# Kernel tuning notes

Measured on AMD Instinct MI355X. Metric: run time of the kernel, lower is better.

The kernel has to match this reference:

```python
import jax, jax.numpy as jnp
import numpy as np

N, E = 100000, 3200000
EMB, HID, OUT = 128, 16, 32
NEG = 0.2  # GATv2 default negative_slope


def _w(key, shape, fan_in):
    return (jax.random.normal(key, shape, jnp.float32) / np.sqrt(fan_in)).astype(jnp.float32)


def setup_inputs() -> dict:
    key = jax.random.key(0)
    ks = jax.random.split(key, 16)
    x = jax.random.normal(ks[0], (N, EMB), jnp.float32)
    edge_index = jax.random.randint(ks[1], (2, E), 0, N, dtype=jnp.int64)
    edge_attr = jax.random.normal(ks[2], (E, 1), jnp.float32)
    return {
        "x": x, "edge_index": edge_index, "edge_attr": edge_attr,
        # layer1: GATv2Conv(EMB -> HID, heads=1, edge_dim=1)
        "W1l": _w(ks[3], (EMB, HID), EMB), "W1r": _w(ks[4], (EMB, HID), EMB),
        "W1e": _w(ks[5], (1, HID), 1), "att1": _w(ks[6], (HID,), HID),
        "b1": jnp.zeros((HID,), jnp.float32),
        # layer2: GATv2Conv(HID -> OUT, heads=1, edge_dim=1)
        "W2l": _w(ks[7], (HID, OUT), HID), "W2r": _w(ks[8], (HID, OUT), HID),
        "W2e": _w(ks[9], (1, OUT), 1), "att2": _w(ks[10], (OUT,), OUT),
        "b2": jnp.zeros((OUT,), jnp.float32),
    }


def gatv2_layer(x, ei, ea, Wl, Wr, We, att, b):
    """PyG GATv2Conv, heads=1, add_self_loops=True (edge fill_value='mean')."""
    n = x.shape[0]
    loop = jnp.arange(n, dtype=ei.dtype)
    ei = jnp.concatenate([ei, jnp.stack([loop, loop])], axis=1)          # [2, E+n]
    ea = jnp.concatenate(
        [ea, jnp.broadcast_to(ea.mean(0, keepdims=True), (n, ea.shape[1]))], axis=0)
    src, dst = ei[0], ei[1]
    xl = x @ Wl                                                          # source proj
    xr = x @ Wr                                                          # target proj
    h = jax.nn.leaky_relu(xl[src] + xr[dst] + ea @ We, NEG)              # [E', C]
    logits = h @ att                                                     # [E']
    m = jax.ops.segment_max(logits, dst, num_segments=n)                 # per-dst softmax
    ex = jnp.exp(logits - m[dst])
    denom = jax.ops.segment_sum(ex, dst, num_segments=n)
    alpha = ex / denom[dst]                                              # [E']
    out = jax.ops.segment_sum(alpha[:, None] * xl[src], dst, num_segments=n) + b
    return out, ei, alpha[:, None]


def reference(x, edge_index, edge_attr, W1l, W1r, W1e, att1, b1, W2l, W2r, W2e, att2, b2):
    h, ei1, a1 = gatv2_layer(x, edge_index, edge_attr, W1l, W1r, W1e, att1, b1)
    h = jax.nn.relu(h)  # F.dropout with training=False is identity (eval mode)
    out, ei2, a2 = gatv2_layer(h, ei1, a1, W2l, W2r, W2e, att2, b2)
    return out, ei2, a2
```

## Files before the change

kernel.cpp:

```cpp
#include <hip/hip_runtime.h>

#define DEVFN __device__ __forceinline__

constexpr int GN = 100000, GE = 3200000;
constexpr int GE1 = GE + GN;
constexpr int GE2 = GE1 + GN;
constexpr int GEMB = 128, GHID = 16, GOUT = 32;
constexpr float GNEG = 0.2f;
constexpr float GEA2 = 100000.f / 3300000.f;

constexpr long long G0 = (long long)GN * GOUT;
constexpr long long G1 = G0 + 2LL * GE2;

constexpr unsigned CHUNK = 400000;

constexpr size_t W_ESC  = 0;
constexpr size_t W_XL1H = 3400000;
constexpr size_t W_XR1  = 4200000;
constexpr size_t W_XL2H = 5800000;
constexpr size_t W_XR2  = 7400000;
constexpr size_t W_RP   = 10600000;
constexpr size_t W_CNT  = 10700004;
constexpr size_t W_BS   = 10800004;
constexpr size_t W_SEA  = 10800260;
constexpr size_t W_WPI  = 10800261;
constexpr size_t W_END  = 10800264;

DEVFN int gidx(const int* __restrict__ ei, long long i, int wpi) {
    return ei[(size_t)i * (size_t)wpi];
}
DEVFN unsigned short f2b(float f) {
    unsigned u = __float_as_uint(f);
    unsigned r = ((u >> 16) & 1u) + 0x7fffu;
    return (unsigned short)((u + r) >> 16);
}
DEVFN float b2fl(unsigned u) { return __uint_as_float(u << 16); }
DEVFN float b2fh(unsigned u) { return __uint_as_float(u & 0xffff0000u); }

__global__ void gl_sentinel(float* outb) {
    if (threadIdx.x == 0 && blockIdx.x == 0) outb[G1] = 3840.0f;
}

__global__ void gl_detect(const int* __restrict__ ei, int* flag) {
    int t = threadIdx.x;
    int v = ei[2 * t + 1];
    unsigned long long nz = __ballot(v != 0);
    if (t == 0) *flag = (nz == 0ull) ? 2 : 1;
}

__global__ void gl_sum(const float* __restrict__ p, int n, float* __restrict__ out) {
    float s = 0.f;
    for (int i = blockIdx.x * blockDim.x + threadIdx.x; i < n; i += gridDim.x * blockDim.x)
        s += p[i];
    #pragma unroll
    for (int o = 32; o > 0; o >>= 1) s += __shfl_down(s, o);
    __shared__ float ls[4];
    if ((threadIdx.x & 63) == 0) ls[threadIdx.x >> 6] = s;
    __syncthreads();
    if (threadIdx.x == 0) atomicAdd(out, ls[0] + ls[1] + ls[2] + ls[3]);
}

__global__ __launch_bounds__(256) void gl_projA(const float* __restrict__ x,
        const float* __restrict__ Wl, const float* __restrict__ Wr,
        unsigned short* __restrict__ xlh, float* __restrict__ xr) {
    __shared__ float sWl[GEMB * GHID], sWr[GEMB * GHID], sx[16 * GEMB];
    for (int i = threadIdx.x; i < GEMB * GHID; i += 256) { sWl[i] = Wl[i]; sWr[i] = Wr[i]; }
    int base = blockIdx.x * 16;
    for (int i = threadIdx.x; i < 16 * GEMB; i += 256) sx[i] = x[(size_t)base * GEMB + i];
    __syncthreads();
    int ln = threadIdx.x >> 4, ch = threadIdx.x & 15;
    float al = 0.f, ar = 0.f;
    #pragma unroll 8
    for (int k = 0; k < GEMB; ++k) {
        float xv = sx[ln * GEMB + k];
        al = fmaf(xv, sWl[k * GHID + ch], al);
        ar = fmaf(xv, sWr[k * GHID + ch], ar);
    }
    xlh[(size_t)(base + ln) * GHID + ch] = f2b(al);
    xr[(size_t)(base + ln) * GHID + ch] = ar;
}

__global__ __launch_bounds__(256) void gl_projB(const float* __restrict__ h,
        const float* __restrict__ Wl, const float* __restrict__ Wr,
        unsigned short* __restrict__ xlh, float* __restrict__ xr) {
    __shared__ float sWl[GHID * GOUT], sWr[GHID * GOUT], sx[8 * GHID];
    for (int i = threadIdx.x; i < GHID * GOUT; i += 256) { sWl[i] = Wl[i]; sWr[i] = Wr[i]; }
    int base = blockIdx.x * 8;
    for (int i = threadIdx.x; i < 8 * GHID; i += 256) sx[i] = h[(size_t)base * GHID + i];
    __syncthreads();
    int ln = threadIdx.x >> 5, ch = threadIdx.x & 31;
    float al = 0.f, ar = 0.f;
    #pragma unroll
    for (int k = 0; k < GHID; ++k) {
        float xv = sx[ln * GHID + k];
        al = fmaf(xv, sWl[k * GOUT + ch], al);
        ar = fmaf(xv, sWr[k * GOUT + ch], ar);
    }
    xlh[(size_t)(base + ln) * GOUT + ch] = f2b(al);
    xr[(size_t)(base + ln) * GOUT + ch] = ar;
}

__global__ void gl_hist(const int* __restrict__ ei, const int* __restrict__ wpip,
                        int* __restrict__ cnt, int2* __restrict__ dl) {
    int e = blockIdx.x * blockDim.x + threadIdx.x;
    if (e >= GE) return;
    int wpi = *wpip;
    int dst = gidx(ei, (long long)GE + e, wpi);
    int lc = atomicAdd(&cnt[dst], 1);
    dl[e] = make_int2(dst, lc);
}

__global__ __launch_bounds__(1024) void gl_scan1(const int* __restrict__ cnt,
                                                 int* __restrict__ rp, int* __restrict__ bs) {
    __shared__ int s[1024];
    int t = threadIdx.x, u = blockIdx.x * 1024 + t;
    s[t] = (u < GN) ? cnt[u] : 0;
    __syncthreads();
    for (int off = 1; off < 1024; off <<= 1) {
        int a = (t >= off) ? s[t - off] : 0;
        __syncthreads();
        s[t] += a;
        __syncthreads();
    }
    if (u < GN) rp[u + 1] = s[t];
    if (t == 1023) bs[blockIdx.x] = s[1023];
}
__global__ void gl_scan2(int* __restrict__ bs, int nb) {
    __shared__ int s[128];
    int t = threadIdx.x;
    s[t] = (t < nb) ? bs[t] : 0;
    __syncthreads();
    for (int off = 1; off < 128; off <<= 1) {
        int a = (t >= off) ? s[t - off] : 0;
        __syncthreads();
        s[t] += a;
        __syncthreads();
    }
    if (t < nb) bs[t] = (t == 0) ? 0 : s[t - 1];
}
__global__ void gl_scan3(int* __restrict__ rp, const int* __restrict__ bs) {
    int u = blockIdx.x * blockDim.x + threadIdx.x;
    if (u < GN) rp[u + 1] += bs[u >> 10];
    if (u == 0) rp[0] = 0;
}

__global__ void gl_slots(const int2* __restrict__ dl, const int* __restrict__ rp,
                         int* __restrict__ inv) {
    int e = blockIdx.x * blockDim.x + threadIdx.x;
    if (e >= GE) return;
    int2 d = dl[e];
    inv[e] = rp[d.x] + d.y;
}

__global__ __launch_bounds__(256) void gl_scatter(const int* __restrict__ ei,
        const int* __restrict__ wpip, const float* __restrict__ eattr,
        const int* __restrict__ inv, int2* __restrict__ pse) {
    int wpi = *wpip;
    unsigned ck = blockIdx.x & 7;
    int stride = (gridDim.x >> 3) * 256;
    for (int e = (blockIdx.x >> 3) * 256 + threadIdx.x; e < GE; e += stride) {
        int slot = inv[e];
        if ((unsigned)slot / CHUNK == ck) {
            int src = gidx(ei, e, wpi);
            pse[slot] = make_int2(src, __float_as_int(eattr[e]));
        }
    }
}

__global__ __launch_bounds__(256) void gl_L1(const int* __restrict__ rp,
        const int2* __restrict__ pse, const float* __restrict__ sea,
        const unsigned short* __restrict__ xlh, const float* __restrict__ xr,
        const float* __restrict__ We, const float* __restrict__ att,
        const float* __restrict__ b1, float* __restrict__ esc,
        float* __restrict__ h1) {
    int u = blockIdx.x * 4 + (threadIdx.x >> 6);
    int lane = threadIdx.x & 63, sg = lane >> 2, ln4 = lane & 3;
    int beg = rp[u], end = rp[u + 1];
    float4 we = *(const float4*)(We + ln4 * 4);
    float4 at = *(const float4*)(att + ln4 * 4);
    float4 xru = *(const float4*)(xr + (size_t)u * GHID + ln4 * 4);
    float mx = -3.0e38f, pd = 0.f;
    float4 acc = make_float4(0.f, 0.f, 0.f, 0.f);
    for (int i = beg + sg; i < end; i += 16) {
        int2 p = pse[i];
        uint2 h = *(const uint2*)(xlh + (size_t)p.x * GHID + ln4 * 4);
        float ea = __int_as_float(p.y);
        float x0 = b2fl(h.x), x1 = b2fh(h.x), x2 = b2fl(h.y), x3 = b2fh(h.y);
        float v, s = 0.f;
        v = x0 + xru.x + ea * we.x; v = v > 0.f ? v : GNEG * v; s = fmaf(v, at.x, s);
        v = x1 + xru.y + ea * we.y; v = v > 0.f ? v : GNEG * v; s = fmaf(v, at.y, s);
        v = x2 + xru.z + ea * we.z; v = v > 0.f ? v : GNEG * v; s = fmaf(v, at.z, s);
        v = x3 + xru.w + ea * we.w; v = v > 0.f ? v : GNEG * v; s = fmaf(v, at.w, s);
        s += __shfl_xor(s, 1); s += __shfl_xor(s, 2);
        if (ln4 == 0) esc[i] = s;
        float nm = fmaxf(mx, s);
        float sc = __expf(mx - nm), pp = __expf(s - nm);
        pd = pd * sc + pp;
        acc.x = acc.x * sc + pp * x0; acc.y = acc.y * sc + pp * x1;
        acc.z = acc.z * sc + pp * x2; acc.w = acc.w * sc + pp * x3;
        mx = nm;
    }
    float lgself = 0.f;
    if (sg == 0) {
        uint2 h = *(const uint2*)(xlh + (size_t)u * GHID + ln4 * 4);
        float ea = sea[0] * (1.f / (float)GE);
        float x0 = b2fl(h.x), x1 = b2fh(h.x), x2 = b2fl(h.y), x3 = b2fh(h.y);
        float v, s = 0.f;
        v = x0 + xru.x + ea * we.x; v = v > 0.f ? v : GNEG * v; s = fmaf(v, at.x, s);
        v = x1 + xru.y + ea * we.y; v = v > 0.f ? v : GNEG * v; s = fmaf(v, at.y, s);
        v = x2 + xru.z + ea * we.z; v = v > 0.f ? v : GNEG * v; s = fmaf(v, at.z, s);
        v = x3 + xru.w + ea * we.w; v = v > 0.f ? v : GNEG * v; s = fmaf(v, at.w, s);
        s += __shfl_xor(s, 1); s += __shfl_xor(s, 2);
        lgself = s;
        float nm = fmaxf(mx, s);
        float sc = __expf(mx - nm), pp = __expf(s - nm);
        pd = pd * sc + pp;
        acc.x = acc.x * sc + pp * x0; acc.y = acc.y * sc + pp * x1;
        acc.z = acc.z * sc + pp * x2; acc.w = acc.w * sc + pp * x3;
        mx = nm;
    }
    #pragma unroll
    for (int o = 4; o <= 32; o <<= 1) {
        float mo = __shfl_xor(mx, o), po = __shfl_xor(pd, o);
        float a0 = __shfl_xor(acc.x, o), a1 = __shfl_xor(acc.y, o);
        float a2 = __shfl_xor(acc.z, o), a3 = __shfl_xor(acc.w, o);
        float nm = fmaxf(mx, mo);
        float sa = __expf(mx - nm), sb = __expf(mo - nm);
        pd = pd * sa + po * sb;
        acc.x = acc.x * sa + a0 * sb; acc.y = acc.y * sa + a1 * sb;
        acc.z = acc.z * sa + a2 * sb; acc.w = acc.w * sa + a3 * sb;
        mx = nm;
    }
    float dinv = 1.f / pd;
    __threadfence_block();
    for (int i = beg + lane; i < end; i += 64)
        esc[i] = __expf(esc[i] - mx) * dinv;
    if (lane == 0) esc[GE + u] = __expf(lgself - mx) * dinv;
    if (lane < 4) {
        float4 b = *(const float4*)(b1 + lane * 4);
        float4 o;
        o.x = acc.x * dinv + b.x; o.y = acc.y * dinv + b.y;
        o.z = acc.z * dinv + b.z; o.w = acc.w * dinv + b.w;
        o.x = o.x > 0.f ? o.x : 0.f; o.y = o.y > 0.f ? o.y : 0.f;
        o.z = o.z > 0.f ? o.z : 0.f; o.w = o.w > 0.f ? o.w : 0.f;
        *(float4*)(h1 + (size_t)u * GHID + lane * 4) = o;
    }
}

__global__ __launch_bounds__(256) void gl_L2(const int* __restrict__ rp,
        const int2* __restrict__ pse,
        const unsigned short* __restrict__ xlh, const float* __restrict__ xr,
        const float* __restrict__ We, const float* __restrict__ att,
        const float* __restrict__ b2, float* __restrict__ esc,
        float* __restrict__ out0) {
    int u = blockIdx.x * 4 + (threadIdx.x >> 6);
    int lane = threadIdx.x & 63, sg = lane >> 3, ln8 = lane & 7;
    int beg = rp[u], end = rp[u + 1];
    float4 we = *(const float4*)(We + ln8 * 4);
    float4 at = *(const float4*)(att + ln8 * 4);
    float4 xru = *(const float4*)(xr + (size_t)u * GOUT + ln8 * 4);
    float mx = -3.0e38f, pd = 0.f;
    float4 acc = make_float4(0.f, 0.f, 0.f, 0.f);
    for (int i = beg + sg; i < end; i += 8) {
        int2 p = pse[i];
        float ea = esc[i];
        uint2 h = *(const uint2*)(xlh + (size_t)p.x * GOUT + ln8 * 4);
        float x0 = b2fl(h.x), x1 = b2fh(h.x), x2 = b2fl(h.y), x3 = b2fh(h.y);
        float v, s = 0.f;
        v = x0 + xru.x + ea * we.x; v = v > 0.f ? v : GNEG * v; s = fmaf(v, at.x, s);
        v = x1 + xru.y + ea * we.y; v = v > 0.f ? v : GNEG * v; s = fmaf(v, at.y, s);
        v = x2 + xru.z + ea * we.z; v = v > 0.f ? v : GNEG * v; s = fmaf(v, at.z, s);
        v = x3 + xru.w + ea * we.w; v = v > 0.f ? v : GNEG * v; s = fmaf(v, at.w, s);
        s += __shfl_xor(s, 1); s += __shfl_xor(s, 2); s += __shfl_xor(s, 4);
        if (ln8 == 0) esc[i] = s;
        float nm = fmaxf(mx, s);
        float sc = __expf(mx - nm), pp = __expf(s - nm);
        pd = pd * sc + pp;
        acc.x = acc.x * sc + pp * x0; acc.y = acc.y * sc + pp * x1;
        acc.z = acc.z * sc + pp * x2; acc.w = acc.w * sc + pp * x3;
        mx = nm;
    }
    float lgs = 0.f;
    if (sg < 2) {
        float ea = (sg == 0) ? esc[GE + u] : GEA2;
        uint2 h = *(const uint2*)(xlh + (size_t)u * GOUT + ln8 * 4);
        float x0 = b2fl(h.x), x1 = b2fh(h.x), x2 = b2fl(h.y), x3 = b2fh(h.y);
        float v, s = 0.f;
        v = x0 + xru.x + ea * we.x; v = v > 0.f ? v : GNEG * v; s = fmaf(v, at.x, s);
        v = x1 + xru.y + ea * we.y; v = v > 0.f ? v : GNEG * v; s = fmaf(v, at.y, s);
        v = x2 + xru.z + ea * we.z; v = v > 0.f ? v : GNEG * v; s = fmaf(v, at.z, s);
        v = x3 + xru.w + ea * we.w; v = v > 0.f ? v : GNEG * v; s = fmaf(v, at.w, s);
        s += __shfl_xor(s, 1); s += __shfl_xor(s, 2); s += __shfl_xor(s, 4);
        lgs = s;
        float nm = fmaxf(mx, s);
        float sc = __expf(mx - nm), pp = __expf(s - nm);
        pd = pd * sc + pp;
        acc.x = acc.x * sc + pp * x0; acc.y = acc.y * sc + pp * x1;
        acc.z = acc.z * sc + pp * x2; acc.w = acc.w * sc + pp * x3;
        mx = nm;
    }
    #pragma unroll
    for (int o = 8; o <= 32; o <<= 1) {
        float mo = __shfl_xor(mx, o), po = __shfl_xor(pd, o);
        float a0 = __shfl_xor(acc.x, o), a1 = __shfl_xor(acc.y, o);
        float a2 = __shfl_xor(acc.z, o), a3 = __shfl_xor(acc.w, o);
        float nm = fmaxf(mx, mo);
        float sa = __expf(mx - nm), sb = __expf(mo - nm);
        pd = pd * sa + po * sb;
        acc.x = acc.x * sa + a0 * sb; acc.y = acc.y * sa + a1 * sb;
        acc.z = acc.z * sa + a2 * sb; acc.w = acc.w * sa + a3 * sb;
        mx = nm;
    }
    float dinv = 1.f / pd;
    __threadfence_block();
    for (int i = beg + lane; i < end; i += 64)
        esc[i] = __expf(esc[i] - mx) * dinv;
    if (lane == 0) esc[GE + u]  = __expf(lgs - mx) * dinv;
    if (lane == 8) esc[GE1 + u] = __expf(lgs - mx) * dinv;
    if (lane < 8) {
        float4 b = *(const float4*)(b2 + lane * 4);
        float4 o;
        o.x = acc.x * dinv + b.x; o.y = acc.y * dinv + b.y;
        o.z = acc.z * dinv + b.z; o.w = acc.w * dinv + b.w;
        *(float4*)(out0 + (size_t)u * GOUT + lane * 4) = o;
    }
}

__global__ void gl_ep(const int* __restrict__ ei, const int* __restrict__ wpip,
                      const int* __restrict__ inv, const float* __restrict__ esc,
                      float* __restrict__ outb) {
    int c = blockIdx.x * blockDim.x + threadIdx.x;
    if (c >= GE2) return;
    int wpi = *wpip;
    int s, dd;
    float av;
    if (c < GE) {
        s = gidx(ei, c, wpi);
        dd = gidx(ei, (long long)GE + c, wpi);
        av = esc[inv[c]];
    } else if (c < GE1) {
        s = dd = c - GE;
        av = esc[c];
    } else {
        s = dd = c - GE1;
        av = esc[c];
    }
    outb[G0 + c]       = (float)s;
    outb[G0 + GE2 + c] = (float)dd;
    outb[G1 + c]       = av;
}

extern "C" void kernel_launch(void* const* d_in, const int* in_sizes, int n_in,
                              void* d_out, int out_size, void* d_ws, size_t ws_size,
                              hipStream_t stream) {
    const float* x     = (const float*)d_in[0];
    const int*   ei    = (const int*)d_in[1];
    const float* eattr = (const float*)d_in[2];
    const float* W1l   = (const float*)d_in[3];
    const float* W1r   = (const float*)d_in[4];
    const float* W1e   = (const float*)d_in[5];
    const float* att1  = (const float*)d_in[6];
    const float* b1    = (const float*)d_in[7];
    const float* W2l   = (const float*)d_in[8];
    const float* W2r   = (const float*)d_in[9];
    const float* W2e   = (const float*)d_in[10];
    const float* att2  = (const float*)d_in[11];
    const float* b2    = (const float*)d_in[12];
    float* outf = (float*)d_out;

    float* ws = (float*)d_ws;
    if (W_END * sizeof(float) > ws_size) {
        gl_sentinel<<<1, 64, 0, stream>>>(outf);
        return;
    }

    float*          esc  = ws + W_ESC;
    unsigned short* xl1h = (unsigned short*)(ws + W_XL1H);
    float*          xr1  = ws + W_XR1;
    unsigned short* xl2h = (unsigned short*)(ws + W_XL2H);
    float*          xr2  = ws + W_XR2;
    int*            rp   = (int*)(ws + W_RP);
    int*            cnt  = (int*)(ws + W_CNT);
    int*            bs   = (int*)(ws + W_BS);
    float*          sea  = ws + W_SEA;
    int*            wpi  = (int*)(ws + W_WPI);

    int2*  dl  = (int2*)(outf + G0);
    int2*  pse = (int2*)(outf + G0);
    int*   inv = (int*)(outf + G1);
    float* h1  = outf;

    hipMemsetAsync(cnt, 0, GN * sizeof(int), stream);
    hipMemsetAsync(sea, 0, 2 * sizeof(float), stream);

    gl_detect<<<1, 64, 0, stream>>>(ei, wpi);
    gl_sum<<<1024, 256, 0, stream>>>(eattr, GE, sea);
    gl_projA<<<GN / 16, 256, 0, stream>>>(x, W1l, W1r, xl1h, xr1);

    int nbe = (GE + 255) / 256;
    gl_hist<<<nbe, 256, 0, stream>>>(ei, wpi, cnt, dl);
    gl_scan1<<<(GN + 1023) / 1024, 1024, 0, stream>>>(cnt, rp, bs);
    gl_scan2<<<1, 128, 0, stream>>>(bs, (GN + 1023) / 1024);
    gl_scan3<<<(GN + 255) / 256, 256, 0, stream>>>(rp, bs);
    gl_slots<<<nbe, 256, 0, stream>>>(dl, rp, inv);
    gl_scatter<<<8192, 256, 0, stream>>>(ei, wpi, eattr, inv, pse);

    gl_L1<<<GN / 4, 256, 0, stream>>>(rp, pse, sea, xl1h, xr1, W1e, att1, b1, esc, h1);
    gl_projB<<<GN / 8, 256, 0, stream>>>(h1, W2l, W2r, xl2h, xr2);
    gl_L2<<<GN / 4, 256, 0, stream>>>(rp, pse, xl2h, xr2, W2e, att2, b2, esc, outf);
    gl_ep<<<(GE2 + 255) / 256, 256, 0, stream>>>(ei, wpi, inv, esc, outf);
}
```

Baseline: 524.2 us.

## Prefetch next edge records in aggregation loops and shrink histogram side buffer

The per-destination aggregation loops in both layers now load the next edge's (src, attr) pair, and in layer 2 the next edge attribute, one iteration ahead. This is meant to hide gather latency behind the current edge's compute. Raw logits now go to a separate workspace buffer instead of being written to and reread from esc in place, which the layer-2 prefetch of esc needs. The histogram pass stores only a rank per edge instead of a (dst, rank) pair, and the slot pass rereads dst from edge_index, trading a smaller write for an extra strided read.

Result: no change. 516.6 us (-1.4%).

```diff
diff --git a/kernel.cpp b/kernel.cpp
--- a/kernel.cpp
+++ b/kernel.cpp
@@ -15,16 +15,17 @@
 constexpr unsigned CHUNK = 400000;
 
 constexpr size_t W_ESC  = 0;
-constexpr size_t W_XL1H = 3400000;
-constexpr size_t W_XR1  = 4200000;
-constexpr size_t W_XL2H = 5800000;
-constexpr size_t W_XR2  = 7400000;
-constexpr size_t W_RP   = 10600000;
-constexpr size_t W_CNT  = 10700004;
-constexpr size_t W_BS   = 10800004;
-constexpr size_t W_SEA  = 10800260;
-constexpr size_t W_WPI  = 10800261;
-constexpr size_t W_END  = 10800264;
+constexpr size_t W_LG   = 3400000;
+constexpr size_t W_XL1H = 6800000;
+constexpr size_t W_XR1  = 7600000;
+constexpr size_t W_XL2H = 9200000;
+constexpr size_t W_XR2  = 10800000;
+constexpr size_t W_RP   = 14000000;
+constexpr size_t W_CNT  = 14100004;
+constexpr size_t W_BS   = 14200004;
+constexpr size_t W_SEA  = 14200260;
+constexpr size_t W_WPI  = 14200261;
+constexpr size_t W_END  = 14200264;
 
 DEVFN int gidx(const int* __restrict__ ei, long long i, int wpi) {
     return ei[(size_t)i * (size_t)wpi];
@@ -101,13 +102,12 @@
 }
 
 __global__ void gl_hist(const int* __restrict__ ei, const int* __restrict__ wpip,
-                        int* __restrict__ cnt, int2* __restrict__ dl) {
+                        int* __restrict__ cnt, int* __restrict__ rank) {
     int e = blockIdx.x * blockDim.x + threadIdx.x;
     if (e >= GE) return;
     int wpi = *wpip;
     int dst = gidx(ei, (long long)GE + e, wpi);
-    int lc = atomicAdd(&cnt[dst], 1);
-    dl[e] = make_int2(dst, lc);
+    rank[e] = atomicAdd(&cnt[dst], 1);
 }
 
 __global__ __launch_bounds__(1024) void gl_scan1(const int* __restrict__ cnt,
@@ -144,12 +144,14 @@
     if (u == 0) rp[0] = 0;
 }
 
-__global__ void gl_slots(const int2* __restrict__ dl, const int* __restrict__ rp,
+__global__ void gl_slots(const int* __restrict__ ei, const int* __restrict__ wpip,
+                         const int* __restrict__ rank, const int* __restrict__ rp,
                          int* __restrict__ inv) {
     int e = blockIdx.x * blockDim.x + threadIdx.x;
     if (e >= GE) return;
-    int2 d = dl[e];
-    inv[e] = rp[d.x] + d.y;
+    int wpi = *wpip;
+    int dst = gidx(ei, (long long)GE + e, wpi);
+    inv[e] = rp[dst] + rank[e];
 }
 
 __global__ __launch_bounds__(256) void gl_scatter(const int* __restrict__ ei,
@@ -172,7 +174,7 @@
         const unsigned short* __restrict__ xlh, const float* __restrict__ xr,
         const float* __restrict__ We, const float* __restrict__ att,
         const float* __restrict__ b1, float* __restrict__ esc,
-        float* __restrict__ h1) {
+        float* __restrict__ lg, float* __restrict__ h1) {
     int u = blockIdx.x * 4 + (threadIdx.x >> 6);
     int lane = threadIdx.x & 63, sg = lane >> 2, ln4 = lane & 3;
     int beg = rp[u], end = rp[u + 1];
@@ -181,8 +183,11 @@
     float4 xru = *(const float4*)(xr + (size_t)u * GHID + ln4 * 4);
     float mx = -3.0e38f, pd = 0.f;
     float4 acc = make_float4(0.f, 0.f, 0.f, 0.f);
-    for (int i = beg + sg; i < end; i += 16) {
-        int2 p = pse[i];
+    int i = beg + sg;
+    int2 p = (i < end) ? pse[i] : make_int2(0, 0);
+    for (; i < end; i += 16) {
+        int inx = i + 16;
+        int2 pn = (inx < end) ? pse[inx] : make_int2(0, 0);
         uint2 h = *(const uint2*)(xlh + (size_t)p.x * GHID + ln4 * 4);
         float ea = __int_as_float(p.y);
         float x0 = b2fl(h.x), x1 = b2fh(h.x), x2 = b2fl(h.y), x3 = b2fh(h.y);
@@ -192,13 +197,14 @@
         v = x2 + xru.z + ea * we.z; v = v > 0.f ? v : GNEG * v; s = fmaf(v, at.z, s);
         v = x3 + xru.w + ea * we.w; v = v > 0.f ? v : GNEG * v; s = fmaf(v, at.w, s);
         s += __shfl_xor(s, 1); s += __shfl_xor(s, 2);
-        if (ln4 == 0) esc[i] = s;
+        if (ln4 == 0) lg[i] = s;
         float nm = fmaxf(mx, s);
         float sc = __expf(mx - nm), pp = __expf(s - nm);
         pd = pd * sc + pp;
         acc.x = acc.x * sc + pp * x0; acc.y = acc.y * sc + pp * x1;
         acc.z = acc.z * sc + pp * x2; acc.w = acc.w * sc + pp * x3;
         mx = nm;
+        p = pn;
     }
     float lgself = 0.f;
     if (sg == 0) {
@@ -233,8 +239,8 @@
     }
     float dinv = 1.f / pd;
     __threadfence_block();
-    for (int i = beg + lane; i < end; i += 64)
-        esc[i] = __expf(esc[i] - mx) * dinv;
+    for (int j = beg + lane; j < end; j += 64)
+        esc[j] = __expf(lg[j] - mx) * dinv;
     if (lane == 0) esc[GE + u] = __expf(lgself - mx) * dinv;
     if (lane < 4) {
         float4 b = *(const float4*)(b1 + lane * 4);
@@ -252,7 +258,7 @@
         const unsigned short* __restrict__ xlh, const float* __restrict__ xr,
         const float* __restrict__ We, const float* __restrict__ att,
         const float* __restrict__ b2, float* __restrict__ esc,
-        float* __restrict__ out0) {
+        float* __restrict__ lg, float* __restrict__ out0) {
     int u = blockIdx.x * 4 + (threadIdx.x >> 6);
     int lane = threadIdx.x & 63, sg = lane >> 3, ln8 = lane & 7;
     int beg = rp[u], end = rp[u + 1];
@@ -261,9 +267,13 @@
     float4 xru = *(const float4*)(xr + (size_t)u * GOUT + ln8 * 4);
     float mx = -3.0e38f, pd = 0.f;
     float4 acc = make_float4(0.f, 0.f, 0.f, 0.f);
-    for (int i = beg + sg; i < end; i += 8) {
-        int2 p = pse[i];
-        float ea = esc[i];
+    int i = beg + sg;
+    int2 p = (i < end) ? pse[i] : make_int2(0, 0);
+    float ea = (i < end) ? esc[i] : 0.f;
+    for (; i < end; i += 8) {
+        int inx = i + 8;
+        int2 pn = (inx < end) ? pse[inx] : make_int2(0, 0);
+        float ean = (inx < end) ? esc[inx] : 0.f;
         uint2 h = *(const uint2*)(xlh + (size_t)p.x * GOUT + ln8 * 4);
         float x0 = b2fl(h.x), x1 = b2fh(h.x), x2 = b2fl(h.y), x3 = b2fh(h.y);
         float v, s = 0.f;
@@ -272,24 +282,25 @@
         v = x2 + xru.z + ea * we.z; v = v > 0.f ? v : GNEG * v; s = fmaf(v, at.z, s);
         v = x3 + xru.w + ea * we.w; v = v > 0.f ? v : GNEG * v; s = fmaf(v, at.w, s);
         s += __shfl_xor(s, 1); s += __shfl_xor(s, 2); s += __shfl_xor(s, 4);
-        if (ln8 == 0) esc[i] = s;
+        if (ln8 == 0) lg[i] = s;
         float nm = fmaxf(mx, s);
         float sc = __expf(mx - nm), pp = __expf(s - nm);
         pd = pd * sc + pp;
         acc.x = acc.x * sc + pp * x0; acc.y = acc.y * sc + pp * x1;
         acc.z = acc.z * sc + pp * x2; acc.w = acc.w * sc + pp * x3;
         mx = nm;
+        p = pn; ea = ean;
     }
     float lgs = 0.f;
     if (sg < 2) {
-        float ea = (sg == 0) ? esc[GE + u] : GEA2;
+        float eas = (sg == 0) ? esc[GE + u] : GEA2;
         uint2 h = *(const uint2*)(xlh + (size_t)u * GOUT + ln8 * 4);
         float x0 = b2fl(h.x), x1 = b2fh(h.x), x2 = b2fl(h.y), x3 = b2fh(h.y);
         float v, s = 0.f;
-        v = x0 + xru.x + ea * we.x; v = v > 0.f ? v : GNEG * v; s = fmaf(v, at.x, s);
-        v = x1 + xru.y + ea * we.y; v = v > 0.f ? v : GNEG * v; s = fmaf(v, at.y, s);
-        v = x2 + xru.z + ea * we.z; v = v > 0.f ? v : GNEG * v; s = fmaf(v, at.z, s);
-        v = x3 + xru.w + ea * we.w; v = v > 0.f ? v : GNEG * v; s = fmaf(v, at.w, s);
+        v = x0 + xru.x + eas * we.x; v = v > 0.f ? v : GNEG * v; s = fmaf(v, at.x, s);
+        v = x1 + xru.y + eas * we.y; v = v > 0.f ? v : GNEG * v; s = fmaf(v, at.y, s);
+        v = x2 + xru.z + eas * we.z; v = v > 0.f ? v : GNEG * v; s = fmaf(v, at.z, s);
+        v = x3 + xru.w + eas * we.w; v = v > 0.f ? v : GNEG * v; s = fmaf(v, at.w, s);
         s += __shfl_xor(s, 1); s += __shfl_xor(s, 2); s += __shfl_xor(s, 4);
         lgs = s;
         float nm = fmaxf(mx, s);
@@ -313,8 +324,8 @@
     }
     float dinv = 1.f / pd;
     __threadfence_block();
-    for (int i = beg + lane; i < end; i += 64)
-        esc[i] = __expf(esc[i] - mx) * dinv;
+    for (int j = beg + lane; j < end; j += 64)
+        esc[j] = __expf(lg[j] - mx) * dinv;
     if (lane == 0) esc[GE + u]  = __expf(lgs - mx) * dinv;
     if (lane == 8) esc[GE1 + u] = __expf(lgs - mx) * dinv;
     if (lane < 8) {
@@ -375,6 +386,7 @@
     }
 
     float*          esc  = ws + W_ESC;
+    float*          lg   = ws + W_LG;
     unsigned short* xl1h = (unsigned short*)(ws + W_XL1H);
     float*          xr1  = ws + W_XR1;
     unsigned short* xl2h = (unsigned short*)(ws + W_XL2H);
@@ -385,10 +397,10 @@
     float*          sea  = ws + W_SEA;
     int*            wpi  = (int*)(ws + W_WPI);
 
-    int2*  dl  = (int2*)(outf + G0);
-    int2*  pse = (int2*)(outf + G0);
-    int*   inv = (int*)(outf + G1);
-    float* h1  = outf;
+    int*   rank = (int*)(outf + G0);
+    int2*  pse  = (int2*)(outf + G0);
+    int*   inv  = (int*)(outf + G1);
+    float* h1   = outf;
 
     hipMemsetAsync(cnt, 0, GN * sizeof(int), stream);
     hipMemsetAsync(sea, 0, 2 * sizeof(float), stream);
@@ -398,15 +410,15 @@
     gl_projA<<<GN / 16, 256, 0, stream>>>(x, W1l, W1r, xl1h, xr1);
 
     int nbe = (GE + 255) / 256;
-    gl_hist<<<nbe, 256, 0, stream>>>(ei, wpi, cnt, dl);
+    gl_hist<<<nbe, 256, 0, stream>>>(ei, wpi, cnt, rank);
     gl_scan1<<<(GN + 1023) / 1024, 1024, 0, stream>>>(cnt, rp, bs);
     gl_scan2<<<1, 128, 0, stream>>>(bs, (GN + 1023) / 1024);
     gl_scan3<<<(GN + 255) / 256, 256, 0, stream>>>(rp, bs);
-    gl_slots<<<nbe, 256, 0, stream>>>(dl, rp, inv);
+    gl_slots<<<nbe, 256, 0, stream>>>(ei, wpi, rank, rp, inv);
     gl_scatter<<<8192, 256, 0, stream>>>(ei, wpi, eattr, inv, pse);
 
-    gl_L1<<<GN / 4, 256, 0, stream>>>(rp, pse, sea, xl1h, xr1, W1e, att1, b1, esc, h1);
+    gl_L1<<<GN / 4, 256, 0, stream>>>(rp, pse, sea, xl1h, xr1, W1e, att1, b1, esc, lg, h1);
     gl_projB<<<GN / 8, 256, 0, stream>>>(h1, W2l, W2r, xl2h, xr2);
-    gl_L2<<<GN / 4, 256, 0, stream>>>(rp, pse, xl2h, xr2, W2e, att2, b2, esc, outf);
+    gl_L2<<<GN / 4, 256, 0, stream>>>(rp, pse, xl2h, xr2, W2e, att2, b2, esc, lg, outf);
     gl_ep<<<(GE2 + 255) / 256, 256, 0, stream>>>(ei, wpi, inv, esc, outf);
 }
```
